# Kernel tuning notes

Hardware: AMD Instinct MI355X
Metric: run time of the kernel (lower is better)

## Reference

```python
import jax, jax.numpy as jnp
import numpy as np
from jax import lax

B, T, E, H, V = 1024, 128, 300, 100, 50000
K = 4  # topk in catch()
NEG_INF = -1e30


def setup_inputs() -> dict:
    key = jax.random.key(0)
    ks = jax.random.split(key, 12)
    word_id = jax.random.randint(ks[0], (B, T), 0, V, dtype=jnp.int32)
    sen_len = jax.random.randint(ks[1], (B,), K, T + 1, dtype=jnp.int32)  # >= K for topk
    label_word_id = jax.random.randint(ks[2], (B, 1), 0, V, dtype=jnp.int32)
    emb = jax.random.normal(ks[3], (V, E), jnp.float32) * 0.1
    W_ih = jax.random.normal(ks[4], (4 * H, E), jnp.float32) * 0.05
    W_hh = jax.random.normal(ks[5], (4 * H, H), jnp.float32) * 0.05
    b_ih = jax.random.normal(ks[6], (4 * H,), jnp.float32) * 0.05
    b_hh = jax.random.normal(ks[7], (4 * H,), jnp.float32) * 0.05
    lin_W = jax.random.normal(ks[8], (6, H), jnp.float32) * 0.1
    lin_b = jax.random.normal(ks[9], (6,), jnp.float32) * 0.1
    ll_W = jax.random.normal(ks[10], (H, E), jnp.float32) * 0.05
    ll_b = jax.random.normal(ks[11], (H,), jnp.float32) * 0.05
    return dict(word_id=word_id, sen_len=sen_len, label_word_id=label_word_id,
                emb=emb, W_ih=W_ih, W_hh=W_hh, b_ih=b_ih, b_hh=b_hh,
                lin_W=lin_W, lin_b=lin_b, ll_W=ll_W, ll_b=ll_b)


def _lstm(x, W_ih, W_hh, b_ih, b_hh):
    # x: (B, T, E) -> out: (B, T, H). Single layer, pytorch gate order i,f,g,o.
    b = b_ih + b_hh
    def step(carry, x_t):
        h, c = carry
        gates = x_t @ W_ih.T + h @ W_hh.T + b  # (B, 4H)
        i, f, g, o = jnp.split(gates, 4, axis=-1)
        c = jax.nn.sigmoid(f) * c + jax.nn.sigmoid(i) * jnp.tanh(g)
        h = jax.nn.sigmoid(o) * jnp.tanh(c)
        return (h, c), h
    h0 = jnp.zeros((x.shape[0], W_hh.shape[1]), x.dtype)
    (_, _), hs = lax.scan(step, (h0, h0), x.transpose(1, 0, 2))
    return hs.transpose(1, 0, 2)


def reference(word_id, sen_len, label_word_id, emb, W_ih, W_hh, b_ih, b_hh,
              lin_W, lin_b, ll_W, ll_b):
    word_vec = emb[word_id]                      # (B, T, E)
    out = _lstm(word_vec, W_ih, W_hh, b_ih, b_hh)  # (B, T, H)

    # last valid hidden state -> linear
    last = out[jnp.arange(out.shape[0]), sen_len - 1]  # (B, H)
    out_f = last @ lin_W.T + lin_b               # (B, 6)

    # label vector through llinear
    label_vec = emb[label_word_id[:, 0]] @ ll_W.T + ll_b  # (B, H)

    # --- catch(), vectorized ---
    scores = jnp.einsum('bth,bh->bt', out, label_vec)     # (B, T)
    valid = jnp.arange(out.shape[1])[None, :] < sen_len[:, None]  # (B, T)
    vals, idx = lax.top_k(jnp.where(valid, scores, NEG_INF), K)   # (B, K)
    s_value = jnp.take_along_axis(out, idx[:, :, None], axis=1)   # (B, K, H)
    pos = jnp.sum(s_value * vals[:, :, None], axis=1)             # (B, H)

    # neg: valid positions excluding topk; original bug: vector_list accumulates
    # across the batch loop -> cumulative sum over batch dimension.
    top_mask = jnp.zeros(valid.shape, bool).at[
        jnp.arange(valid.shape[0])[:, None], idx].set(True)
    neg_mask = valid & ~top_mask                                   # (B, T)
    per_neg = jnp.einsum('bth,bt->bh', out, neg_mask.astype(out.dtype))
    neg = jnp.cumsum(per_neg, axis=0)                              # (B, H)

    l_rep = pos @ lin_W.T + lin_b
    r_rep = neg @ lin_W.T + lin_b
    return (out_f, l_rep, r_rep)
```

## Files before the change

### kernel.cpp

```cpp
#include <hip/hip_runtime.h>
#include <hip/hip_bf16.h>
#include <cstdint>

#define Bn   1024
#define Tn   128
#define En   300
#define Hn   100
#define Vn   50000
#define G4n  400
#define MPn  50048
#define NPn  448

typedef __bf16 bf16x8 __attribute__((ext_vector_type(8)));
typedef _Float16 half8 __attribute__((ext_vector_type(8)));
typedef _Float16 half2v __attribute__((ext_vector_type(2)));
typedef float  f32x4  __attribute__((ext_vector_type(4)));

#define OFF_TABLE  0ull
#define OFF_WFRAG  44800000ull
#define OFF_WFRAGB 44914688ull
#define OFF_LLWT   45201408ull
#define OFF_LV     45321408ull
#define OFF_PN6    45731008ull

__device__ __forceinline__ float sigf(float x) {
    return __builtin_amdgcn_rcpf(1.0f + __expf(-x));
}
__device__ __forceinline__ float tanhfast(float x) {
    return 1.0f - 2.0f * __builtin_amdgcn_rcpf(__expf(2.0f * x) + 1.0f);
}

#define BAR_LDS() do {                                         \
    asm volatile("s_waitcnt lgkmcnt(0)" ::: "memory");          \
    __builtin_amdgcn_s_barrier();                               \
    asm volatile("" ::: "memory");                              \
} while (0)

__global__ void k_prep(const float* __restrict__ W_ih, const float* __restrict__ W_hh,
                       const float* __restrict__ llW,
                       uint4* __restrict__ wfrag, uint4* __restrict__ wfragB,
                       float* __restrict__ llwt) {
    int idx = blockIdx.x * 256 + threadIdx.x;
    if (idx < 28 * 4 * 64) {
        int lane = idx & 63, tk = idx >> 6;
        int nt = tk >> 2, kc = tk & 3;
        int n = nt * 16 + (lane & 15);
        int k0 = kc * 32 + (lane >> 4) * 8;
        int q = n & 3, u = n >> 2;
        union { _Float16 h[8]; uint4 v; } pk;
#pragma unroll
        for (int j = 0; j < 8; j++) {
            int k = k0 + j;
            pk.h[j] = (_Float16)((u < Hn && k < Hn) ? W_hh[(size_t)(q * Hn + u) * Hn + k] : 0.0f);
        }
        wfrag[idx] = pk.v;
    }
    if (idx < 10 * 28 * 64) {
        int lane = idx & 63, tk = idx >> 6;
        int kc = tk / 28, nsg = tk - kc * 28;
        int n = nsg * 16 + (lane & 15);
        int k0 = kc * 32 + (lane >> 4) * 8;
        int q = n & 3, u = n >> 2;
        union { __bf16 h[8]; uint4 v; } pk;
#pragma unroll
        for (int j = 0; j < 8; j++) {
            int k = k0 + j;
            pk.h[j] = (__bf16)((u < Hn && k < En) ? W_ih[(size_t)(q * Hn + u) * En + k] : 0.0f);
        }
        wfragB[idx] = pk.v;
    }
    if (idx < En * Hn) {
        int k = idx / Hn, h = idx - k * Hn;
        llwt[idx] = llW[(size_t)h * En + k];
    }
}

__global__ __launch_bounds__(256, 2) void k_table(
    const float* __restrict__ emb, const uint4* __restrict__ wfragB,
    const float* __restrict__ b_ih, const float* __restrict__ b_hh,
    _Float16* __restrict__ table) {
    __shared__ __bf16 a_sh[64][328];
    const int tid = threadIdx.x;
    const int mt = blockIdx.x >> 1, nh = blockIdx.x & 1;

#pragma unroll
    for (int it = 0; it < 5; it++) {
        int x = it * 256 + tid;
        int row = x / 20, seg = x - row * 20;
        int gr = mt * 64 + row;
        const float* ar = emb + (size_t)(gr < Vn ? gr : Vn - 1) * En;
        int c0 = seg * 16;
        union { __bf16 h[16]; bf16x8 v[2]; } pk;
#pragma unroll
        for (int g = 0; g < 4; g++) {
            int c = c0 + g * 4;
            if (c + 4 <= En) {
                float4 f = *(const float4*)(ar + c);
                pk.h[g * 4 + 0] = (__bf16)f.x; pk.h[g * 4 + 1] = (__bf16)f.y;
                pk.h[g * 4 + 2] = (__bf16)f.z; pk.h[g * 4 + 3] = (__bf16)f.w;
            } else {
                pk.h[g * 4 + 0] = (__bf16)0.f; pk.h[g * 4 + 1] = (__bf16)0.f;
                pk.h[g * 4 + 2] = (__bf16)0.f; pk.h[g * 4 + 3] = (__bf16)0.f;
            }
        }
        *(bf16x8*)&a_sh[row][c0] = pk.v[0];
        *(bf16x8*)&a_sh[row][c0 + 8] = pk.v[1];
    }
    __syncthreads();

    const int wv = tid >> 6, l = tid & 63;
    const int c16 = l & 15, quad = l >> 4;
    f32x4 acc[14];
#pragma unroll
    for (int i = 0; i < 14; i++) acc[i] = (f32x4){0.f, 0.f, 0.f, 0.f};

    uint4 bcur[14];
#pragma unroll
    for (int ns = 0; ns < 14; ns++) bcur[ns] = wfragB[((0 * 28 + nh * 14 + ns) << 6) + l];

    for (int kc = 0; kc < 10; kc++) {
        uint4 bnxt[14];
        if (kc < 9) {
#pragma unroll
            for (int ns = 0; ns < 14; ns++) bnxt[ns] = wfragB[(((kc + 1) * 28 + nh * 14 + ns) << 6) + l];
        }
        bf16x8 af = *(const bf16x8*)&a_sh[wv * 16 + c16][kc * 32 + quad * 8];
#pragma unroll
        for (int ns = 0; ns < 14; ns++)
            acc[ns] = __builtin_amdgcn_mfma_f32_16x16x32_bf16(af, __builtin_bit_cast(bf16x8, bcur[ns]), acc[ns], 0, 0, 0);
        if (kc < 9) {
#pragma unroll
            for (int ns = 0; ns < 14; ns++) bcur[ns] = bnxt[ns];
        }
    }
#pragma unroll
    for (int ns = 0; ns < 14; ns++) {
        int n = (nh * 14 + ns) * 16 + c16;
        int q = n & 3, u = n >> 2;
        if (u < Hn) {
            int j = q * Hn + u;
            float bias = b_ih[j] + b_hh[j];
#pragma unroll
            for (int r = 0; r < 4; r++) {
                int m = mt * 64 + wv * 16 + quad * 4 + r;
                if (m < Vn) table[(size_t)m * NPn + n] = (_Float16)(acc[ns][r] + bias);
            }
        }
    }
}

__global__ void k_label(const int* __restrict__ lwid, const float* __restrict__ emb,
                        const float* __restrict__ llwt, const float* __restrict__ llb,
                        float* __restrict__ lv) {
    __shared__ float er[En];
    __shared__ float part[Hn];
    int b = blockIdx.x;
    int lid = lwid[b];
    for (int k = threadIdx.x; k < En; k += 256) er[k] = emb[(size_t)lid * En + k];
    __syncthreads();
    int h = threadIdx.x & 127, half = threadIdx.x >> 7;
    float acc = 0.f;
    if (h < Hn) {
        int k0 = half * 150, k1 = k0 + 150;
        for (int k = k0; k < k1; k++) acc += er[k] * llwt[k * Hn + h];
        if (half == 1) part[h] = acc;
    }
    __syncthreads();
    if (h < Hn && half == 0) lv[(size_t)b * Hn + h] = acc + part[h] + llb[h];
}

__global__ __launch_bounds__(512, 2) void k_lstm(
    const int* __restrict__ word_id, const int* __restrict__ sen_len,
    const _Float16* __restrict__ table, const uint4* __restrict__ wfrag,
    const float* __restrict__ lv, const float* __restrict__ linW,
    const float* __restrict__ linb, float* __restrict__ pn6,
    float* __restrict__ d_out) {
    __shared__ __align__(16) _Float16 h_cur[2][4][144];
    __shared__ __align__(16) _Float16 oh_lds[4][12832];
    __shared__ __align__(16) float    spw[4][Tn][8];
    __shared__ int      widc[4][Tn];
    __shared__ float    pos_sh[4][Hn];
    __shared__ float    lasth_sh[4][Hn];
    __shared__ float    neg_sh[4][Hn];
    __shared__ float    tk_val[4][4];
    __shared__ int      tk_idx[4][4];

    const int tid = threadIdx.x;
    const int w = tid >> 6, l = tid & 63;
    const int c16 = l & 15, quad = l >> 4;
    const int b0 = blockIdx.x * 4;

    for (int i = tid; i < 576; i += 512) ((uint32_t*)h_cur)[i] = 0u;
    { int imb = tid >> 7, it = tid & 127; widc[imb][it] = word_id[(b0 + imb) * Tn + it] * NPn; }

    const bool has4 = (w == 0);
    const int TB = has4 ? 0 : 4 + 3 * (w - 1);
    const int NT = has4 ? 4 : 3;

    half8 bfr[4][4];
#pragma unroll
    for (int kc = 0; kc < 4; kc++) {
        bfr[0][kc] = __builtin_bit_cast(half8, wfrag[((TB + 0) * 4 + kc) * 64 + l]);
        bfr[1][kc] = __builtin_bit_cast(half8, wfrag[((TB + 1) * 4 + kc) * 64 + l]);
        bfr[2][kc] = __builtin_bit_cast(half8, wfrag[((TB + 2) * 4 + kc) * 64 + l]);
        if (has4) bfr[3][kc] = __builtin_bit_cast(half8, wfrag[((TB + 3) * 4 + kc) * 64 + l]);
    }

    const int mb = c16 & 3, dup = c16 >> 2;
    const bool act = (dup < NT);
    const int u = (TB + dup) * 4 + quad;
    const int slen = act ? sen_len[b0 + mb] : 0;
    const float lt_reg = act ? lv[(size_t)(b0 + mb) * Hn + u] : 0.f;
    const _Float16* tb_u = table + u * 4;

    __syncthreads();

    uint2 xq = {0, 0}, xq1 = {0, 0};
    if (act) {
        xq  = *(const uint2*)(tb_u + (size_t)widc[mb][0]);
        xq1 = *(const uint2*)(tb_u + (size_t)widc[mb][1]);
    }

    float c_reg = 0.f, sumh = 0.f, lasth = 0.f;
    float p_carry = 0.f;

    for (int t = 0; t < Tn; t++) {
        const _Float16* hp = &h_cur[t & 1][0][0];
        half8 hf0 = *(const half8*)(hp + (c16 & 3) * 144 + 0 * 32 + quad * 8);
        half8 hf1 = *(const half8*)(hp + (c16 & 3) * 144 + 1 * 32 + quad * 8);
        half8 hf2 = *(const half8*)(hp + (c16 & 3) * 144 + 2 * 32 + quad * 8);
        half8 hf3 = *(const half8*)(hp + (c16 & 3) * 144 + 3 * 32 + quad * 8);
        f32x4 acc0, acc1, acc2, acc3;
        acc0 = __builtin_amdgcn_mfma_f32_16x16x32_f16(bfr[0][0], hf0, (f32x4){0.f, 0.f, 0.f, 0.f}, 0, 0, 0);
        acc1 = __builtin_amdgcn_mfma_f32_16x16x32_f16(bfr[1][0], hf0, (f32x4){0.f, 0.f, 0.f, 0.f}, 0, 0, 0);
        acc2 = __builtin_amdgcn_mfma_f32_16x16x32_f16(bfr[2][0], hf0, (f32x4){0.f, 0.f, 0.f, 0.f}, 0, 0, 0);
        if (has4) acc3 = __builtin_amdgcn_mfma_f32_16x16x32_f16(bfr[3][0], hf0, (f32x4){0.f, 0.f, 0.f, 0.f}, 0, 0, 0);
        acc0 = __builtin_amdgcn_mfma_f32_16x16x32_f16(bfr[0][1], hf1, acc0, 0, 0, 0);
        acc1 = __builtin_amdgcn_mfma_f32_16x16x32_f16(bfr[1][1], hf1, acc1, 0, 0, 0);
        acc2 = __builtin_amdgcn_mfma_f32_16x16x32_f16(bfr[2][1], hf1, acc2, 0, 0, 0);
        if (has4) acc3 = __builtin_amdgcn_mfma_f32_16x16x32_f16(bfr[3][1], hf1, acc3, 0, 0, 0);
        acc0 = __builtin_amdgcn_mfma_f32_16x16x32_f16(bfr[0][2], hf2, acc0, 0, 0, 0);
        acc1 = __builtin_amdgcn_mfma_f32_16x16x32_f16(bfr[1][2], hf2, acc1, 0, 0, 0);
        acc2 = __builtin_amdgcn_mfma_f32_16x16x32_f16(bfr[2][2], hf2, acc2, 0, 0, 0);
        if (has4) acc3 = __builtin_amdgcn_mfma_f32_16x16x32_f16(bfr[3][2], hf2, acc3, 0, 0, 0);
        acc0 = __builtin_amdgcn_mfma_f32_16x16x32_f16(bfr[0][3], hf3, acc0, 0, 0, 0);
        acc1 = __builtin_amdgcn_mfma_f32_16x16x32_f16(bfr[1][3], hf3, acc1, 0, 0, 0);
        acc2 = __builtin_amdgcn_mfma_f32_16x16x32_f16(bfr[2][3], hf3, acc2, 0, 0, 0);
        if (has4) acc3 = __builtin_amdgcn_mfma_f32_16x16x32_f16(bfr[3][3], hf3, acc3, 0, 0, 0);
        {
            float pr = p_carry;
            pr += __shfl_xor(pr, 4, 64);
            pr += __shfl_xor(pr, 8, 64);
            pr += __shfl_xor(pr, 16, 64);
            pr += __shfl_xor(pr, 32, 64);
            if (l < 4 && t > 0) spw[l][t - 1][w] = pr;
        }
        f32x4 g = acc0;
        g = (dup == 1) ? acc1 : g;
        g = (dup == 2) ? acc2 : g;
        if (has4) g = (dup == 3) ? acc3 : g;
        float p = 0.f;
        if (act) {
            half2v x01 = __builtin_bit_cast(half2v, xq.x);
            half2v x23 = __builtin_bit_cast(half2v, xq.y);
            float gi = g[0] + (float)x01.x;
            float gf = g[1] + (float)x01.y;
            float gg = g[2] + (float)x23.x;
            float go = g[3] + (float)x23.y;
            float c = sigf(gf) * c_reg + sigf(gi) * tanhfast(gg);
            c_reg = c;
            float hh = sigf(go) * tanhfast(c);
            _Float16 h16 = (_Float16)hh;
            h_cur[(t + 1) & 1][mb][u] = h16;
            oh_lds[mb][t * Hn + u] = h16;
            if (t < slen) sumh += hh;
            if (t == slen - 1) lasth = hh;
            p = hh * lt_reg;
            int tn2 = (t + 2 < Tn) ? t + 2 : Tn - 1;
            xq = xq1;
            xq1 = *(const uint2*)(tb_u + (size_t)widc[mb][tn2]);
        }
        p_carry = p;
        BAR_LDS();
    }
    {
        float pr = p_carry;
        pr += __shfl_xor(pr, 4, 64);
        pr += __shfl_xor(pr, 8, 64);
        pr += __shfl_xor(pr, 16, 64);
        pr += __shfl_xor(pr, 32, 64);
        if (l < 4) spw[l][Tn - 1][w] = pr;
    }
    __syncthreads();
    if (w < 4) {
        int sl = sen_len[b0 + w];
        float4 a0 = *(const float4*)&spw[w][l][0];
        float4 a1 = *(const float4*)&spw[w][l][4];
        float4 c0 = *(const float4*)&spw[w][l + 64][0];
        float4 c1 = *(const float4*)&spw[w][l + 64][4];
        float sa = (a0.x + a0.y + a0.z + a0.w) + (a1.x + a1.y + a1.z + a1.w);
        float sb = (c0.x + c0.y + c0.z + c0.w) + (c1.x + c1.y + c1.z + c1.w);
        float s0 = (l < sl) ? sa : -1e30f;
        float s1 = (l + 64 < sl) ? sb : -1e30f;
        bool tk0 = false, tk1 = false;
#pragma unroll
        for (int p4 = 0; p4 < 4; p4++) {
            float v = tk0 ? -1e30f : s0;
            int ix = l;
            float v1 = tk1 ? -1e30f : s1;
            if (v1 > v) { v = v1; ix = l + 64; }
            for (int off = 32; off; off >>= 1) {
                float ov = __shfl_down(v, off, 64);
                int oi = __shfl_down(ix, off, 64);
                if (ov > v || (ov == v && oi < ix)) { v = ov; ix = oi; }
            }
            v = __shfl(v, 0, 64);
            ix = __shfl(ix, 0, 64);
            if (l == 0) { tk_val[w][p4] = v; tk_idx[w][p4] = ix; }
            if (ix == l) tk0 = true;
            if (ix == l + 64) tk1 = true;
        }
    }
    __syncthreads();
    if (act) {
        float pos = 0.f, nsum = sumh;
#pragma unroll
        for (int p4 = 0; p4 < 4; p4++) {
            int ix = tk_idx[mb][p4];
            float r = (float)oh_lds[mb][ix * Hn + u];
            pos += tk_val[mb][p4] * r;
            nsum -= r;
        }
        pos_sh[mb][u] = pos;
        lasth_sh[mb][u] = lasth;
        neg_sh[mb][u] = nsum;
    }
    __syncthreads();
    if (tid < 72) {
        int which = tid / 24, r = tid - which * 24;
        int pmb = r / 6, o = r - pmb * 6;
        const float* src = (which == 0) ? &lasth_sh[pmb][0]
                         : (which == 1) ? &pos_sh[pmb][0] : &neg_sh[pmb][0];
        float acc2 = (which == 2) ? 0.f : linb[o];
        for (int uu = 0; uu < Hn; uu++) acc2 += src[uu] * linW[o * Hn + uu];
        if (which == 0)      d_out[(b0 + pmb) * 6 + o] = acc2;
        else if (which == 1) d_out[Bn * 6 + (b0 + pmb) * 6 + o] = acc2;
        else                 pn6[(b0 + pmb) * 6 + o] = acc2;
    }
}

__global__ __launch_bounds__(1024) void k_scan6(const float* __restrict__ pn6,
                                                const float* __restrict__ linb,
                                                float* __restrict__ d_out) {
    __shared__ float wsum[16];
    __shared__ float wpre[16];
    int o = blockIdx.x, t = threadIdx.x;
    int lane = t & 63, wv = t >> 6;
    float v = pn6[t * 6 + o];
#pragma unroll
    for (int off = 1; off < 64; off <<= 1) {
        float x = __shfl_up(v, off, 64);
        if (lane >= off) v += x;
    }
    if (lane == 63) wsum[wv] = v;
    __syncthreads();
    if (t < 16) {
        float s = wsum[t];
#pragma unroll
        for (int off = 1; off < 16; off <<= 1) {
            float x = __shfl_up(s, off, 64);
            if (t >= off) s += x;
        }
        wpre[t] = s;
    }
    __syncthreads();
    float pre = wv ? wpre[wv - 1] : 0.f;
    d_out[2 * Bn * 6 + t * 6 + o] = v + pre + linb[o];
}

extern "C" void kernel_launch(void* const* d_in, const int* in_sizes, int n_in,
                              void* d_out, int out_size, void* d_ws, size_t ws_size,
                              hipStream_t stream) {
    const int*   word_id = (const int*)d_in[0];
    const int*   sen_len = (const int*)d_in[1];
    const int*   lwid    = (const int*)d_in[2];
    const float* emb     = (const float*)d_in[3];
    const float* W_ih    = (const float*)d_in[4];
    const float* W_hh    = (const float*)d_in[5];
    const float* b_ih    = (const float*)d_in[6];
    const float* b_hh    = (const float*)d_in[7];
    const float* linW    = (const float*)d_in[8];
    const float* linb    = (const float*)d_in[9];
    const float* llW     = (const float*)d_in[10];
    const float* llb     = (const float*)d_in[11];

    char* ws = (char*)d_ws;
    _Float16* table  = (_Float16*)(ws + OFF_TABLE);
    uint4*    wfrag  = (uint4*)(ws + OFF_WFRAG);
    uint4*    wfragB = (uint4*)(ws + OFF_WFRAGB);
    float*    llwt   = (float*)(ws + OFF_LLWT);
    float*    lvp    = (float*)(ws + OFF_LV);
    float*    pn6    = (float*)(ws + OFF_PN6);
    float*    outp   = (float*)d_out;

    k_prep<<<118, 256, 0, stream>>>(W_ih, W_hh, llW, wfrag, wfragB, llwt);
    k_table<<<(MPn / 64) * 2, 256, 0, stream>>>(emb, wfragB, b_ih, b_hh, table);
    k_label<<<Bn, 256, 0, stream>>>(lwid, emb, llwt, llb, lvp);
    k_lstm<<<Bn / 4, 512, 0, stream>>>(word_id, sen_len, table, wfrag, lvp, linW, linb, pn6, outp);
    k_scan6<<<6, 1024, 0, stream>>>(pn6, linb, outp);
}
```

Before: 269.6 us.

## Fuse label projection into LSTM kernel and use DPP/swizzle score reductions

Drops the separate k_label kernel and the llW transpose from k_prep. Each active LSTM lane now computes its own label-vector element with a float4 dot product over emb and llW before the recurrence. This removes one launch and a global round trip, at the cost of extra startup work per block. The per-step score reduction swaps four shfl_xor operations for two DPP row shifts and one ds_swizzle, which leaves two partial sums per wave, so the spw buffer is widened to 16 columns.

```diff
diff --git a/kernel.cpp b/kernel.cpp
--- a/kernel.cpp
+++ b/kernel.cpp
@@ -19,9 +19,7 @@
 #define OFF_TABLE  0ull
 #define OFF_WFRAG  44800000ull
 #define OFF_WFRAGB 44914688ull
-#define OFF_LLWT   45201408ull
-#define OFF_LV     45321408ull
-#define OFF_PN6    45731008ull
+#define OFF_PN6    45201408ull
 
 __device__ __forceinline__ float sigf(float x) {
     return __builtin_amdgcn_rcpf(1.0f + __expf(-x));
@@ -36,10 +34,14 @@
     asm volatile("" ::: "memory");                              \
 } while (0)
 
+#define DPP_ADD_SHL(v, N) do {                                                     \
+    int _s = __builtin_amdgcn_update_dpp(0, __builtin_bit_cast(int, (v)),          \
+                                         0x100 | (N), 0xF, 0xF, true);             \
+    (v) += __builtin_bit_cast(float, _s);                                          \
+} while (0)
+
 __global__ void k_prep(const float* __restrict__ W_ih, const float* __restrict__ W_hh,
-                       const float* __restrict__ llW,
-                       uint4* __restrict__ wfrag, uint4* __restrict__ wfragB,
-                       float* __restrict__ llwt) {
+                       uint4* __restrict__ wfrag, uint4* __restrict__ wfragB) {
     int idx = blockIdx.x * 256 + threadIdx.x;
     if (idx < 28 * 4 * 64) {
         int lane = idx & 63, tk = idx >> 6;
@@ -68,10 +70,6 @@
             pk.h[j] = (__bf16)((u < Hn && k < En) ? W_ih[(size_t)(q * Hn + u) * En + k] : 0.0f);
         }
         wfragB[idx] = pk.v;
-    }
-    if (idx < En * Hn) {
-        int k = idx / Hn, h = idx - k * Hn;
-        llwt[idx] = llW[(size_t)h * En + k];
     }
 }
 
@@ -149,35 +147,16 @@
     }
 }
 
-__global__ void k_label(const int* __restrict__ lwid, const float* __restrict__ emb,
-                        const float* __restrict__ llwt, const float* __restrict__ llb,
-                        float* __restrict__ lv) {
-    __shared__ float er[En];
-    __shared__ float part[Hn];
-    int b = blockIdx.x;
-    int lid = lwid[b];
-    for (int k = threadIdx.x; k < En; k += 256) er[k] = emb[(size_t)lid * En + k];
-    __syncthreads();
-    int h = threadIdx.x & 127, half = threadIdx.x >> 7;
-    float acc = 0.f;
-    if (h < Hn) {
-        int k0 = half * 150, k1 = k0 + 150;
-        for (int k = k0; k < k1; k++) acc += er[k] * llwt[k * Hn + h];
-        if (half == 1) part[h] = acc;
-    }
-    __syncthreads();
-    if (h < Hn && half == 0) lv[(size_t)b * Hn + h] = acc + part[h] + llb[h];
-}
-
 __global__ __launch_bounds__(512, 2) void k_lstm(
     const int* __restrict__ word_id, const int* __restrict__ sen_len,
+    const int* __restrict__ lwid, const float* __restrict__ emb,
+    const float* __restrict__ llW, const float* __restrict__ llb,
     const _Float16* __restrict__ table, const uint4* __restrict__ wfrag,
-    const float* __restrict__ lv, const float* __restrict__ linW,
-    const float* __restrict__ linb, float* __restrict__ pn6,
-    float* __restrict__ d_out) {
+    const float* __restrict__ linW, const float* __restrict__ linb,
+    float* __restrict__ pn6, float* __restrict__ d_out) {
     __shared__ __align__(16) _Float16 h_cur[2][4][144];
     __shared__ __align__(16) _Float16 oh_lds[4][12832];
-    __shared__ __align__(16) float    spw[4][Tn][8];
+    __shared__ __align__(16) float    spw[4][Tn][16];
     __shared__ int      widc[4][Tn];
     __shared__ float    pos_sh[4][Hn];
     __shared__ float    lasth_sh[4][Hn];
@@ -210,8 +189,22 @@
     const bool act = (dup < NT);
     const int u = (TB + dup) * 4 + quad;
     const int slen = act ? sen_len[b0 + mb] : 0;
-    const float lt_reg = act ? lv[(size_t)(b0 + mb) * Hn + u] : 0.f;
     const _Float16* tb_u = table + u * 4;
+
+    float lt_reg = 0.f;
+    if (act) {
+        const int lid = lwid[b0 + mb];
+        const float* er = emb + (size_t)lid * En;
+        const float* wr = llW + (size_t)u * En;
+        float sx = 0.f, sy = 0.f, sz = 0.f, sw = 0.f;
+        for (int k = 0; k < En; k += 4) {
+            float4 e = *(const float4*)(er + k);
+            float4 ww = *(const float4*)(wr + k);
+            sx += e.x * ww.x; sy += e.y * ww.y;
+            sz += e.z * ww.z; sw += e.w * ww.w;
+        }
+        lt_reg = (sx + sy) + (sz + sw) + llb[u];
+    }
 
     __syncthreads();
 
@@ -249,11 +242,12 @@
         if (has4) acc3 = __builtin_amdgcn_mfma_f32_16x16x32_f16(bfr[3][3], hf3, acc3, 0, 0, 0);
         {
             float pr = p_carry;
-            pr += __shfl_xor(pr, 4, 64);
-            pr += __shfl_xor(pr, 8, 64);
-            pr += __shfl_xor(pr, 16, 64);
-            pr += __shfl_xor(pr, 32, 64);
-            if (l < 4 && t > 0) spw[l][t - 1][w] = pr;
+            DPP_ADD_SHL(pr, 4);
+            DPP_ADD_SHL(pr, 8);
+            int sw_ = __builtin_amdgcn_ds_swizzle(__builtin_bit_cast(int, pr), 0x401F);
+            pr += __builtin_bit_cast(float, sw_);
+            if (c16 < 4 && (quad & 1) == 0 && t > 0)
+                spw[c16][t - 1][w * 2 + (quad >> 1)] = pr;
         }
         f32x4 g = acc0;
         g = (dup == 1) ? acc1 : g;
@@ -285,21 +279,28 @@
     }
     {
         float pr = p_carry;
-        pr += __shfl_xor(pr, 4, 64);
-        pr += __shfl_xor(pr, 8, 64);
-        pr += __shfl_xor(pr, 16, 64);
-        pr += __shfl_xor(pr, 32, 64);
-        if (l < 4) spw[l][Tn - 1][w] = pr;
+        DPP_ADD_SHL(pr, 4);
+        DPP_ADD_SHL(pr, 8);
+        int sw_ = __builtin_amdgcn_ds_swizzle(__builtin_bit_cast(int, pr), 0x401F);
+        pr += __builtin_bit_cast(float, sw_);
+        if (c16 < 4 && (quad & 1) == 0)
+            spw[c16][Tn - 1][w * 2 + (quad >> 1)] = pr;
     }
     __syncthreads();
     if (w < 4) {
         int sl = sen_len[b0 + w];
         float4 a0 = *(const float4*)&spw[w][l][0];
         float4 a1 = *(const float4*)&spw[w][l][4];
+        float4 a2 = *(const float4*)&spw[w][l][8];
+        float4 a3 = *(const float4*)&spw[w][l][12];
         float4 c0 = *(const float4*)&spw[w][l + 64][0];
         float4 c1 = *(const float4*)&spw[w][l + 64][4];
-        float sa = (a0.x + a0.y + a0.z + a0.w) + (a1.x + a1.y + a1.z + a1.w);
-        float sb = (c0.x + c0.y + c0.z + c0.w) + (c1.x + c1.y + c1.z + c1.w);
+        float4 c2 = *(const float4*)&spw[w][l + 64][8];
+        float4 c3 = *(const float4*)&spw[w][l + 64][12];
+        float sa = ((a0.x + a0.y + a0.z + a0.w) + (a1.x + a1.y + a1.z + a1.w))
+                 + ((a2.x + a2.y + a2.z + a2.w) + (a3.x + a3.y + a3.z + a3.w));
+        float sb = ((c0.x + c0.y + c0.z + c0.w) + (c1.x + c1.y + c1.z + c1.w))
+                 + ((c2.x + c2.y + c2.z + c2.w) + (c3.x + c3.y + c3.z + c3.w));
         float s0 = (l < sl) ? sa : -1e30f;
         float s1 = (l + 64 < sl) ? sb : -1e30f;
         bool tk0 = false, tk1 = false;
@@ -398,14 +399,12 @@
     _Float16* table  = (_Float16*)(ws + OFF_TABLE);
     uint4*    wfrag  = (uint4*)(ws + OFF_WFRAG);
     uint4*    wfragB = (uint4*)(ws + OFF_WFRAGB);
-    float*    llwt   = (float*)(ws + OFF_LLWT);
-    float*    lvp    = (float*)(ws + OFF_LV);
     float*    pn6    = (float*)(ws + OFF_PN6);
     float*    outp   = (float*)d_out;
 
-    k_prep<<<118, 256, 0, stream>>>(W_ih, W_hh, llW, wfrag, wfragB, llwt);
+    k_prep<<<70, 256, 0, stream>>>(W_ih, W_hh, wfrag, wfragB);
     k_table<<<(MPn / 64) * 2, 256, 0, stream>>>(emb, wfragB, b_ih, b_hh, table);
-    k_label<<<Bn, 256, 0, stream>>>(lwid, emb, llwt, llb, lvp);
-    k_lstm<<<Bn / 4, 512, 0, stream>>>(word_id, sen_len, table, wfrag, lvp, linW, linb, pn6, outp);
+    k_lstm<<<Bn / 4, 512, 0, stream>>>(word_id, sen_len, lwid, emb, llW, llb,
+                                       table, wfrag, linW, linb, pn6, outp);
     k_scan6<<<6, 1024, 0, stream>>>(pn6, linb, outp);
 }
```

Result: no change. 270.0 us (+0.1%).

## Pack 16 sequences per LSTM block and spill hidden history to global

Applied to the files above, without the earlier changes.

Reworks the LSTM kernel so each 256-thread block handles 16 batch rows instead of 4, using all 16 MFMA columns for distinct sequences rather than duplicating gate tiles. Each wave now owns 6-7 gate tiles and computes several hidden units per lane, which cuts the number of blocks to 64 and removes wasted MFMA work. The per-step hidden history moves from LDS to a global workspace buffer that is read back for the top-k gather. The risk is that 64 blocks leave most CUs idle, and the serial per-step chain per block gets longer.

```diff
diff --git a/kernel.cpp b/kernel.cpp
--- a/kernel.cpp
+++ b/kernel.cpp
@@ -22,6 +22,7 @@
 #define OFF_LLWT   45201408ull
 #define OFF_LV     45321408ull
 #define OFF_PN6    45731008ull
+#define OFF_OHG    45755584ull
 
 __device__ __forceinline__ float sigf(float x) {
     return __builtin_amdgcn_rcpf(1.0f + __expf(-x));
@@ -169,137 +170,150 @@
     if (h < Hn && half == 0) lv[(size_t)b * Hn + h] = acc + part[h] + llb[h];
 }
 
-__global__ __launch_bounds__(512, 2) void k_lstm(
+__global__ __launch_bounds__(256, 1) void k_lstm(
     const int* __restrict__ word_id, const int* __restrict__ sen_len,
     const _Float16* __restrict__ table, const uint4* __restrict__ wfrag,
     const float* __restrict__ lv, const float* __restrict__ linW,
-    const float* __restrict__ linb, float* __restrict__ pn6,
-    float* __restrict__ d_out) {
-    __shared__ __align__(16) _Float16 h_cur[2][4][144];
-    __shared__ __align__(16) _Float16 oh_lds[4][12832];
-    __shared__ __align__(16) float    spw[4][Tn][8];
-    __shared__ int      widc[4][Tn];
-    __shared__ float    pos_sh[4][Hn];
-    __shared__ float    lasth_sh[4][Hn];
-    __shared__ float    neg_sh[4][Hn];
-    __shared__ float    tk_val[4][4];
-    __shared__ int      tk_idx[4][4];
+    const float* __restrict__ linb, _Float16* __restrict__ ohg,
+    float* __restrict__ pn6, float* __restrict__ d_out) {
+    __shared__ __align__(16) _Float16 h_cur[2][16][136];
+    __shared__ __align__(16) float    spw[16][Tn][4];
+    __shared__ int      widc[16][Tn];
+    __shared__ float    pos_sh[16][Hn];
+    __shared__ float    lasth_sh[16][Hn];
+    __shared__ float    neg_sh[16][Hn];
+    __shared__ float    tk_val[16][4];
+    __shared__ int      tk_idx[16][4];
 
     const int tid = threadIdx.x;
     const int w = tid >> 6, l = tid & 63;
     const int c16 = l & 15, quad = l >> 4;
-    const int b0 = blockIdx.x * 4;
-
-    for (int i = tid; i < 576; i += 512) ((uint32_t*)h_cur)[i] = 0u;
-    { int imb = tid >> 7, it = tid & 127; widc[imb][it] = word_id[(b0 + imb) * Tn + it] * NPn; }
-
-    const bool has4 = (w == 0);
-    const int TB = has4 ? 0 : 4 + 3 * (w - 1);
-    const int NT = has4 ? 4 : 3;
-
-    half8 bfr[4][4];
+    const int b0 = blockIdx.x * 16;
+
+    for (int i = tid; i < 2176; i += 256) ((uint32_t*)h_cur)[i] = 0u;
+    for (int i = tid; i < 2048; i += 256)
+        widc[i >> 7][i & 127] = word_id[(b0 + (i >> 7)) * Tn + (i & 127)] * NPn;
+
+    const bool has7 = (w == 0);
+    const int TB = has7 ? 0 : 7 + 6 * (w - 1);
+    const int NT = has7 ? 7 : 6;
+#define IF_ITEM(i) if ((i) < 6 || has7)
+
+    half8 bfr[7][4];
 #pragma unroll
     for (int kc = 0; kc < 4; kc++) {
-        bfr[0][kc] = __builtin_bit_cast(half8, wfrag[((TB + 0) * 4 + kc) * 64 + l]);
-        bfr[1][kc] = __builtin_bit_cast(half8, wfrag[((TB + 1) * 4 + kc) * 64 + l]);
-        bfr[2][kc] = __builtin_bit_cast(half8, wfrag[((TB + 2) * 4 + kc) * 64 + l]);
-        if (has4) bfr[3][kc] = __builtin_bit_cast(half8, wfrag[((TB + 3) * 4 + kc) * 64 + l]);
-    }
-
-    const int mb = c16 & 3, dup = c16 >> 2;
-    const bool act = (dup < NT);
-    const int u = (TB + dup) * 4 + quad;
-    const int slen = act ? sen_len[b0 + mb] : 0;
-    const float lt_reg = act ? lv[(size_t)(b0 + mb) * Hn + u] : 0.f;
-    const _Float16* tb_u = table + u * 4;
-
-    __syncthreads();
-
-    uint2 xq = {0, 0}, xq1 = {0, 0};
-    if (act) {
-        xq  = *(const uint2*)(tb_u + (size_t)widc[mb][0]);
-        xq1 = *(const uint2*)(tb_u + (size_t)widc[mb][1]);
-    }
-
-    float c_reg = 0.f, sumh = 0.f, lasth = 0.f;
+#pragma unroll
+        for (int i = 0; i < 6; i++)
+            bfr[i][kc] = __builtin_bit_cast(half8, wfrag[((TB + i) * 4 + kc) * 64 + l]);
+        bfr[6][kc] = has7 ? __builtin_bit_cast(half8, wfrag[((TB + 6) * 4 + kc) * 64 + l])
+                          : bfr[5][kc];
+    }
+
+    const int bat = c16;
+    const int slen = sen_len[b0 + bat];
+    int u4o[7], u16o[7], uho[7];
+    float lt[7];
+#pragma unroll
+    for (int i = 0; i < 7; i++) {
+        int ui = (TB + i) * 4 + quad;
+        u4o[i] = ui * 4; u16o[i] = ui * 16; uho[i] = bat * 136 + ui;
+        lt[i] = 0.f;
+        IF_ITEM(i) lt[i] = lv[(size_t)(b0 + bat) * Hn + ui];
+    }
+
+    __syncthreads();
+
+    uint2 xq[7], xq1[7];
+    {
+        int w0o = widc[bat][0], w1o = widc[bat][1];
+#pragma unroll
+        for (int i = 0; i < 7; i++) {
+            xq[i] = (uint2){0, 0}; xq1[i] = (uint2){0, 0};
+            IF_ITEM(i) {
+                xq[i]  = *(const uint2*)(table + w0o + u4o[i]);
+                xq1[i] = *(const uint2*)(table + w1o + u4o[i]);
+            }
+        }
+    }
+
+    float creg[7], sumh[7], lastv[7];
+#pragma unroll
+    for (int i = 0; i < 7; i++) { creg[i] = 0.f; sumh[i] = 0.f; lastv[i] = 0.f; }
     float p_carry = 0.f;
+    _Float16* ohg_t = ohg + (size_t)blockIdx.x * Tn * 1600;
 
     for (int t = 0; t < Tn; t++) {
-        const _Float16* hp = &h_cur[t & 1][0][0];
-        half8 hf0 = *(const half8*)(hp + (c16 & 3) * 144 + 0 * 32 + quad * 8);
-        half8 hf1 = *(const half8*)(hp + (c16 & 3) * 144 + 1 * 32 + quad * 8);
-        half8 hf2 = *(const half8*)(hp + (c16 & 3) * 144 + 2 * 32 + quad * 8);
-        half8 hf3 = *(const half8*)(hp + (c16 & 3) * 144 + 3 * 32 + quad * 8);
-        f32x4 acc0, acc1, acc2, acc3;
-        acc0 = __builtin_amdgcn_mfma_f32_16x16x32_f16(bfr[0][0], hf0, (f32x4){0.f, 0.f, 0.f, 0.f}, 0, 0, 0);
-        acc1 = __builtin_amdgcn_mfma_f32_16x16x32_f16(bfr[1][0], hf0, (f32x4){0.f, 0.f, 0.f, 0.f}, 0, 0, 0);
-        acc2 = __builtin_amdgcn_mfma_f32_16x16x32_f16(bfr[2][0], hf0, (f32x4){0.f, 0.f, 0.f, 0.f}, 0, 0, 0);
-        if (has4) acc3 = __builtin_amdgcn_mfma_f32_16x16x32_f16(bfr[3][0], hf0, (f32x4){0.f, 0.f, 0.f, 0.f}, 0, 0, 0);
-        acc0 = __builtin_amdgcn_mfma_f32_16x16x32_f16(bfr[0][1], hf1, acc0, 0, 0, 0);
-        acc1 = __builtin_amdgcn_mfma_f32_16x16x32_f16(bfr[1][1], hf1, acc1, 0, 0, 0);
-        acc2 = __builtin_amdgcn_mfma_f32_16x16x32_f16(bfr[2][1], hf1, acc2, 0, 0, 0);
-        if (has4) acc3 = __builtin_amdgcn_mfma_f32_16x16x32_f16(bfr[3][1], hf1, acc3, 0, 0, 0);
-        acc0 = __builtin_amdgcn_mfma_f32_16x16x32_f16(bfr[0][2], hf2, acc0, 0, 0, 0);
-        acc1 = __builtin_amdgcn_mfma_f32_16x16x32_f16(bfr[1][2], hf2, acc1, 0, 0, 0);
-        acc2 = __builtin_amdgcn_mfma_f32_16x16x32_f16(bfr[2][2], hf2, acc2, 0, 0, 0);
-        if (has4) acc3 = __builtin_amdgcn_mfma_f32_16x16x32_f16(bfr[3][2], hf2, acc3, 0, 0, 0);
-        acc0 = __builtin_amdgcn_mfma_f32_16x16x32_f16(bfr[0][3], hf3, acc0, 0, 0, 0);
-        acc1 = __builtin_amdgcn_mfma_f32_16x16x32_f16(bfr[1][3], hf3, acc1, 0, 0, 0);
-        acc2 = __builtin_amdgcn_mfma_f32_16x16x32_f16(bfr[2][3], hf3, acc2, 0, 0, 0);
-        if (has4) acc3 = __builtin_amdgcn_mfma_f32_16x16x32_f16(bfr[3][3], hf3, acc3, 0, 0, 0);
+        const _Float16* hp = &h_cur[t & 1][0][0] + bat * 136;
+        half8 hf0 = *(const half8*)(hp + 0 * 32 + quad * 8);
+        half8 hf1 = *(const half8*)(hp + 1 * 32 + quad * 8);
+        half8 hf2 = *(const half8*)(hp + 2 * 32 + quad * 8);
+        half8 hf3 = *(const half8*)(hp + 3 * 32 + quad * 8);
+        f32x4 acc[7];
+#pragma unroll
+        for (int i = 0; i < 7; i++) {
+            IF_ITEM(i) {
+                acc[i] = __builtin_amdgcn_mfma_f32_16x16x32_f16(bfr[i][0], hf0, (f32x4){0.f, 0.f, 0.f, 0.f}, 0, 0, 0);
+                acc[i] = __builtin_amdgcn_mfma_f32_16x16x32_f16(bfr[i][1], hf1, acc[i], 0, 0, 0);
+                acc[i] = __builtin_amdgcn_mfma_f32_16x16x32_f16(bfr[i][2], hf2, acc[i], 0, 0, 0);
+                acc[i] = __builtin_amdgcn_mfma_f32_16x16x32_f16(bfr[i][3], hf3, acc[i], 0, 0, 0);
+            } else acc[i] = (f32x4){0.f, 0.f, 0.f, 0.f};
+        }
         {
             float pr = p_carry;
-            pr += __shfl_xor(pr, 4, 64);
-            pr += __shfl_xor(pr, 8, 64);
             pr += __shfl_xor(pr, 16, 64);
             pr += __shfl_xor(pr, 32, 64);
-            if (l < 4 && t > 0) spw[l][t - 1][w] = pr;
-        }
-        f32x4 g = acc0;
-        g = (dup == 1) ? acc1 : g;
-        g = (dup == 2) ? acc2 : g;
-        if (has4) g = (dup == 3) ? acc3 : g;
+            if (quad == 0 && t > 0) spw[bat][t - 1][w] = pr;
+        }
         float p = 0.f;
-        if (act) {
-            half2v x01 = __builtin_bit_cast(half2v, xq.x);
-            half2v x23 = __builtin_bit_cast(half2v, xq.y);
-            float gi = g[0] + (float)x01.x;
-            float gf = g[1] + (float)x01.y;
-            float gg = g[2] + (float)x23.x;
-            float go = g[3] + (float)x23.y;
-            float c = sigf(gf) * c_reg + sigf(gi) * tanhfast(gg);
-            c_reg = c;
-            float hh = sigf(go) * tanhfast(c);
-            _Float16 h16 = (_Float16)hh;
-            h_cur[(t + 1) & 1][mb][u] = h16;
-            oh_lds[mb][t * Hn + u] = h16;
-            if (t < slen) sumh += hh;
-            if (t == slen - 1) lasth = hh;
-            p = hh * lt_reg;
+        _Float16* oh_row = ohg_t;
+#pragma unroll
+        for (int i = 0; i < 7; i++) {
+            IF_ITEM(i) {
+                half2v x01 = __builtin_bit_cast(half2v, xq[i].x);
+                half2v x23 = __builtin_bit_cast(half2v, xq[i].y);
+                float gi = acc[i][0] + (float)x01.x;
+                float gf = acc[i][1] + (float)x01.y;
+                float gg = acc[i][2] + (float)x23.x;
+                float go = acc[i][3] + (float)x23.y;
+                float c = sigf(gf) * creg[i] + sigf(gi) * tanhfast(gg);
+                creg[i] = c;
+                float hh = sigf(go) * tanhfast(c);
+                _Float16 h16 = (_Float16)hh;
+                h_cur[(t + 1) & 1][0][uho[i]] = h16;
+                oh_row[u16o[i] + bat] = h16;
+                if (t < slen) sumh[i] += hh;
+                if (t == slen - 1) lastv[i] = hh;
+                p += hh * lt[i];
+            }
+        }
+        {
             int tn2 = (t + 2 < Tn) ? t + 2 : Tn - 1;
-            xq = xq1;
-            xq1 = *(const uint2*)(tb_u + (size_t)widc[mb][tn2]);
+            int wno = widc[bat][tn2];
+#pragma unroll
+            for (int i = 0; i < 7; i++) {
+                xq[i] = xq1[i];
+                IF_ITEM(i) xq1[i] = *(const uint2*)(table + wno + u4o[i]);
+            }
         }
         p_carry = p;
+        ohg_t += 1600;
         BAR_LDS();
     }
     {
         float pr = p_carry;
-        pr += __shfl_xor(pr, 4, 64);
-        pr += __shfl_xor(pr, 8, 64);
         pr += __shfl_xor(pr, 16, 64);
         pr += __shfl_xor(pr, 32, 64);
-        if (l < 4) spw[l][Tn - 1][w] = pr;
-    }
-    __syncthreads();
-    if (w < 4) {
-        int sl = sen_len[b0 + w];
-        float4 a0 = *(const float4*)&spw[w][l][0];
-        float4 a1 = *(const float4*)&spw[w][l][4];
-        float4 c0 = *(const float4*)&spw[w][l + 64][0];
-        float4 c1 = *(const float4*)&spw[w][l + 64][4];
-        float sa = (a0.x + a0.y + a0.z + a0.w) + (a1.x + a1.y + a1.z + a1.w);
-        float sb = (c0.x + c0.y + c0.z + c0.w) + (c1.x + c1.y + c1.z + c1.w);
+        if (quad == 0) spw[bat][Tn - 1][w] = pr;
+    }
+    __syncthreads();
+    const _Float16* oh_gb = ohg + (size_t)blockIdx.x * Tn * 1600;
+    for (int j = 0; j < 4; j++) {
+        int kb = w * 4 + j;
+        int sl = sen_len[b0 + kb];
+        float4 a0 = *(const float4*)&spw[kb][l][0];
+        float4 c0 = *(const float4*)&spw[kb][l + 64][0];
+        float sa = (a0.x + a0.y) + (a0.z + a0.w);
+        float sb = (c0.x + c0.y) + (c0.z + c0.w);
         float s0 = (l < sl) ? sa : -1e30f;
         float s1 = (l + 64 < sl) ? sb : -1e30f;
         bool tk0 = false, tk1 = false;
@@ -316,28 +330,37 @@
             }
             v = __shfl(v, 0, 64);
             ix = __shfl(ix, 0, 64);
-            if (l == 0) { tk_val[w][p4] = v; tk_idx[w][p4] = ix; }
+            if (l == 0) { tk_val[kb][p4] = v; tk_idx[kb][p4] = ix; }
             if (ix == l) tk0 = true;
             if (ix == l + 64) tk1 = true;
         }
     }
     __syncthreads();
-    if (act) {
-        float pos = 0.f, nsum = sumh;
-#pragma unroll
-        for (int p4 = 0; p4 < 4; p4++) {
-            int ix = tk_idx[mb][p4];
-            float r = (float)oh_lds[mb][ix * Hn + u];
-            pos += tk_val[mb][p4] * r;
-            nsum -= r;
-        }
-        pos_sh[mb][u] = pos;
-        lasth_sh[mb][u] = lasth;
-        neg_sh[mb][u] = nsum;
-    }
-    __syncthreads();
-    if (tid < 72) {
-        int which = tid / 24, r = tid - which * 24;
+    {
+        int ix0 = tk_idx[bat][0] * 1600, ix1 = tk_idx[bat][1] * 1600;
+        int ix2 = tk_idx[bat][2] * 1600, ix3 = tk_idx[bat][3] * 1600;
+        float v0 = tk_val[bat][0], v1 = tk_val[bat][1];
+        float v2 = tk_val[bat][2], v3 = tk_val[bat][3];
+#pragma unroll
+        for (int i = 0; i < 7; i++) {
+            IF_ITEM(i) {
+                int uo = u16o[i] + bat;
+                float r0 = (float)oh_gb[ix0 + uo];
+                float r1 = (float)oh_gb[ix1 + uo];
+                float r2 = (float)oh_gb[ix2 + uo];
+                float r3 = (float)oh_gb[ix3 + uo];
+                float pos = v0 * r0 + v1 * r1 + v2 * r2 + v3 * r3;
+                float nsum = sumh[i] - ((r0 + r1) + (r2 + r3));
+                int ui = u4o[i] >> 2;
+                pos_sh[bat][ui] = pos;
+                lasth_sh[bat][ui] = lastv[i];
+                neg_sh[bat][ui] = nsum;
+            }
+        }
+    }
+    __syncthreads();
+    for (int x = tid; x < 288; x += 256) {
+        int which = x / 96, r = x - which * 96;
         int pmb = r / 6, o = r - pmb * 6;
         const float* src = (which == 0) ? &lasth_sh[pmb][0]
                          : (which == 1) ? &pos_sh[pmb][0] : &neg_sh[pmb][0];
@@ -347,6 +370,7 @@
         else if (which == 1) d_out[Bn * 6 + (b0 + pmb) * 6 + o] = acc2;
         else                 pn6[(b0 + pmb) * 6 + o] = acc2;
     }
+#undef IF_ITEM
 }
 
 __global__ __launch_bounds__(1024) void k_scan6(const float* __restrict__ pn6,
@@ -401,11 +425,13 @@
     float*    llwt   = (float*)(ws + OFF_LLWT);
     float*    lvp    = (float*)(ws + OFF_LV);
     float*    pn6    = (float*)(ws + OFF_PN6);
+    _Float16* ohg    = (_Float16*)(ws + OFF_OHG);
     float*    outp   = (float*)d_out;
 
     k_prep<<<118, 256, 0, stream>>>(W_ih, W_hh, llW, wfrag, wfragB, llwt);
     k_table<<<(MPn / 64) * 2, 256, 0, stream>>>(emb, wfragB, b_ih, b_hh, table);
     k_label<<<Bn, 256, 0, stream>>>(lwid, emb, llwt, llb, lvp);
-    k_lstm<<<Bn / 4, 512, 0, stream>>>(word_id, sen_len, table, wfrag, lvp, linW, linb, pn6, outp);
+    k_lstm<<<Bn / 16, 256, 0, stream>>>(word_id, sen_len, table, wfrag, lvp,
+                                        linW, linb, ohg, pn6, outp);
     k_scan6<<<6, 1024, 0, stream>>>(pn6, linb, outp);
 }
```

Result: slower. 407.7 us (+51.2%).
